# Performance work log

Hardware: AMD Instinct MI355X
Metric: run time of the kernel (lower is better)

## Reference

```python
import jax, jax.numpy as jnp
import numpy as np

B, H, W, C, F = 32, 32, 32, 256, 64
K_NEIGH = 32  # L1 pixel-distance cutoff used for the static mask


def _distance_mask(h, w, k):
    # coords: [hw, 2] of (y, x); L1 pixel distances, normalized by max(h, w)
    ys, xs = jnp.meshgrid(jnp.arange(h), jnp.arange(w), indexing='ij')
    coords = jnp.stack([ys, xs], axis=-1).reshape(-1, 2).astype(jnp.float32)
    diff = jnp.abs(coords[:, None, :] - coords[None, :, :]).sum(-1)  # [hw, hw], == cdist p=1
    dist = diff / float(max(h, w))
    return jnp.where(diff <= k, dist, 0.0)


def setup_inputs() -> dict:
    key = jax.random.key(0)
    ks = jax.random.split(key, 7)
    return {
        'feature_map': jax.random.normal(ks[0], (B, H, W, C), dtype=jnp.float32),
        'emb_W': jax.random.normal(ks[1], (F, C), dtype=jnp.float32) * (1.0 / np.sqrt(C)),
        'emb_b': jax.random.normal(ks[2], (F,), dtype=jnp.float32) * 0.01,
        'attn_W': jax.random.normal(ks[3], (C, C), dtype=jnp.float32) * (1.0 / np.sqrt(C)),
        'attn_b': jax.random.normal(ks[4], (C,), dtype=jnp.float32) * 0.01,
        'thr_W': jax.random.normal(ks[5], (1, C), dtype=jnp.float32) * (1.0 / np.sqrt(C)),
        'thr_b': jax.random.normal(ks[6], (1,), dtype=jnp.float32) * 0.01,
        'layer': 0,
    }


def reference(feature_map, emb_W, emb_b, attn_W, attn_b, thr_W, thr_b, layer):
    b, h, w, c = feature_map.shape
    hw = h * w
    x = feature_map.reshape(b, hw, c)  # row-major (y, x) flatten, matches torch view

    # 1x1 conv -> per-pixel linear: instance embeddings [b, hw, F]
    emb = jnp.einsum('bnc,fc->bnf', x, emb_W) + emb_b

    # squared Euclidean pairwise distances (cdist p=2, then squared)
    sq = jnp.sum(emb * emb, axis=-1)  # [b, hw]
    d2 = jnp.maximum(sq[:, :, None] + sq[:, None, :]
                     - 2.0 * jnp.einsum('bnf,bmf->bnm', emb, emb), 0.0)

    mask = _distance_mask(h, w, K_NEIGH)  # [hw, hw] static buffer
    sim = jax.nn.softmax(jnp.exp(-d2) - (1.0 - mask), axis=-1)  # [b, hw, hw]

    # shortcut = attention_conv(feature_map): [b, hw, c]
    shortcut = jnp.einsum('bnc,dc->bnd', x, attn_W) + attn_b

    # per-pixel learned threshold: [b, hw]
    Tinst = (jnp.einsum('bnc,oc->bno', shortcut, thr_W) + thr_b)[..., 0]

    A = jax.nn.softmax(jnp.maximum(sim - Tinst[:, None, :], 0.0), axis=-1)

    # bmm: out[b, i, c] = sum_j shortcut[b, j, c] * A[b, i, j]
    attn_out = jnp.einsum('bjc,bij->bic', shortcut, A)

    res = (x + attn_out).reshape(b, h, w, c)
    return res
```

## Files before the change

kernel.cpp:

```cpp
#include <hip/hip_runtime.h>
#include <hip/hip_bf16.h>


typedef short bf16x8 __attribute__((ext_vector_type(8)));
typedef float f32x4 __attribute__((ext_vector_type(4)));

#define LOG2E 1.4426950408889634f

__device__ __forceinline__ unsigned short f2bf(float f) {
  unsigned u = __float_as_uint(f);
  u += 0x7fffu + ((u >> 16) & 1u);
  return (unsigned short)(u >> 16);
}
__device__ __forceinline__ float bf2f(unsigned short h) {
  return __uint_as_float(((unsigned)h) << 16);
}
__device__ __forceinline__ unsigned pack2(float a, float b) {
  return (unsigned)f2bf(a) | ((unsigned)f2bf(b) << 16);
}
__device__ __forceinline__ unsigned cvtpk(float lo, float hi) {
  unsigned r;
  asm("v_cvt_pk_bf16_f32 %0, %1, %2" : "=v"(r) : "v"(lo), "v"(hi));
  return r;
}
__device__ __forceinline__ float exp2x(float x) {
  float r;
  asm("v_exp_f32 %0, %1" : "=v"(r) : "v"(x));
  return r;
}
__device__ __forceinline__ f32x4 mfma16(bf16x8 a, bf16x8 b, f32x4 c) {
  return __builtin_amdgcn_mfma_f32_16x16x32_bf16(a, b, c, 0, 0, 0);
}
__device__ __forceinline__ int iabs(int v) { return v < 0 ? -v : v; }
__device__ __forceinline__ void load_lds16(const void* g, void* l) {
  __builtin_amdgcn_global_load_lds(
      (const __attribute__((address_space(1))) unsigned int*)g,
      (__attribute__((address_space(3))) unsigned int*)l, 16, 0, 0);
}

__device__ __forceinline__ float e_chain(float g, float nsq2i, float sq2j,
                                         int diff) {
  float w2 = fminf(fmaf(2.f * LOG2E, g, nsq2i - sq2j), 0.f);
  float fd = (float)diff;
  float fs = (diff <= 32) ? fd : 0.f;
  return exp2x(fmaf(exp2x(w2), LOG2E, fmaf(fs, LOG2E / 32.f, -LOG2E)));
}

__global__ __launch_bounds__(256) void k_prep(const float* __restrict__ embW,
                                              const float* __restrict__ attnW,
                                              unsigned short* __restrict__ Wb) {
  const int i = (blockIdx.x * 256 + threadIdx.x) * 4;
  float4 v = (i < 16384) ? *(const float4*)(embW + i)
                         : *(const float4*)(attnW + (i - 16384));
  ushort4 p; p.x = f2bf(v.x); p.y = f2bf(v.y); p.z = f2bf(v.z); p.w = f2bf(v.w);
  *(ushort4*)(Wb + i) = p;
}

__global__ __launch_bounds__(256) void k_lin(const float* __restrict__ x,
                                             const unsigned short* __restrict__ Wb,
                                             const float* __restrict__ embB,
                                             const float* __restrict__ attnB,
                                             const float* __restrict__ thrW,
                                             const float* __restrict__ thrB,
                                             unsigned short* __restrict__ embb,
                                             float* __restrict__ sq2,
                                             unsigned short* __restrict__ scT,
                                             float* __restrict__ T2out) {
  __shared__ union {
    struct { unsigned short xs[64][40]; unsigned short ws[320][40]; } a;
    unsigned short St[256][72];
  } sm;
  const int t = threadIdx.x;
  const int Mbase = blockIdx.x * 64;
  const int lane = t & 63, wave = t >> 6;
  const int wm = wave >> 1, wn = wave & 1;
  const int l15 = lane & 15, quad = lane >> 4;

  f32x4 acc[2][10] = {};
  for (int k0 = 0; k0 < 256; k0 += 32) {
    {
      int row = t >> 2, c0 = (t & 3) * 8;
      const float* src = x + (size_t)(Mbase + row) * 256 + k0 + c0;
      float4 a = *(const float4*)src;
      float4 b = *(const float4*)(src + 4);
      uint4 p; p.x = pack2(a.x, a.y); p.y = pack2(a.z, a.w);
      p.z = pack2(b.x, b.y); p.w = pack2(b.z, b.w);
      *(uint4*)&sm.a.xs[row][c0] = p;
    }
    {
      const unsigned short* wsrc = Wb + (size_t)t * 256 + k0;
      for (int s = 0; s < 4; s++)
        *(uint4*)&sm.a.ws[t][s * 8] = *(const uint4*)(wsrc + s * 8);
      if (t < 64) {
        const unsigned short* wsrc2 = Wb + (size_t)(256 + t) * 256 + k0;
        for (int s = 0; s < 4; s++)
          *(uint4*)&sm.a.ws[256 + t][s * 8] = *(const uint4*)(wsrc2 + s * 8);
      }
    }
    __syncthreads();
    bf16x8 af[2];
    af[0] = *(const bf16x8*)&sm.a.xs[wm * 32 + l15][quad * 8];
    af[1] = *(const bf16x8*)&sm.a.xs[wm * 32 + 16 + l15][quad * 8];
    for (int nt = 0; nt < 10; nt++) {
      bf16x8 bfr = *(const bf16x8*)&sm.a.ws[wn * 160 + nt * 16 + l15][quad * 8];
      acc[0][nt] = mfma16(af[0], bfr, acc[0][nt]);
      acc[1][nt] = mfma16(af[1], bfr, acc[1][nt]);
    }
    __syncthreads();
  }

  if (wn == 0) {
    float sp[2][4] = {{0.f,0.f,0.f,0.f},{0.f,0.f,0.f,0.f}};
    for (int rt = 0; rt < 2; rt++)
      for (int nt = 0; nt < 4; nt++) {
        int n = nt * 16 + l15;
        float bias = embB[n];
        for (int r = 0; r < 4; r++) {
          float v = acc[rt][nt][r] + bias;
          unsigned short hb = f2bf(v);
          int row = wm * 32 + rt * 16 + quad * 4 + r;
          embb[(size_t)(Mbase + row) * 64 + n] = hb;
          float vf = bf2f(hb);
          sp[rt][r] += vf * vf;
        }
      }
    for (int m = 8; m >= 1; m >>= 1)
      for (int rt = 0; rt < 2; rt++)
        for (int r = 0; r < 4; r++)
          sp[rt][r] += __shfl_xor(sp[rt][r], m);
    if (l15 == 0)
      for (int rt = 0; rt < 2; rt++)
        for (int r = 0; r < 4; r++)
          sq2[Mbase + wm * 32 + rt * 16 + quad * 4 + r] = sp[rt][r] * LOG2E;
  }

  for (int rt = 0; rt < 2; rt++)
    for (int nt = 0; nt < 10; nt++) {
      int n = wn * 160 + nt * 16 + l15;
      if (n < 64) continue;
      int c = n - 64;
      float bias = attnB[c];
      for (int r = 0; r < 4; r++) {
        float v = acc[rt][nt][r] + bias;
        sm.St[c][wm * 32 + rt * 16 + quad * 4 + r] = f2bf(v);
      }
    }
  __syncthreads();

  const int b = Mbase >> 10, jbase = Mbase & 1023;
  {
    unsigned short* dst = scT + ((size_t)b * 256 + t) * 1024 + jbase;
    for (int s = 0; s < 8; s++)
      *(uint4*)(dst + s * 8) = *(const uint4*)&sm.St[t][s * 8];
  }
  {
    float tp = 0.f;
    int j = t >> 2, cs = (t & 3) * 64;
    for (int c = 0; c < 64; c++)
      tp += bf2f(sm.St[cs + c][j]) * thrW[cs + c];
    tp += __shfl_xor(tp, 1);
    tp += __shfl_xor(tp, 2);
    if ((t & 3) == 0) T2out[Mbase + j] = (tp + thrB[0]) * LOG2E;
  }
}

__global__ __launch_bounds__(256) void k_out2(const unsigned short* __restrict__ embb,
                                              const float* __restrict__ sq2,
                                              const float* __restrict__ T2,
                                              const unsigned short* __restrict__ scT,
                                              const float* __restrict__ x,
                                              float* __restrict__ out) {
  __shared__ unsigned short Kb[2][32 * 64];
  __shared__ unsigned short Sb[2][1024 * 8];
  __shared__ unsigned short Pb[2][64 * 40];
  __shared__ float zbuf[64];
  const int t = threadIdx.x, lane = t & 63, w = t >> 6;
  const int l15 = lane & 15, quad = lane >> 4;
  const int b = blockIdx.x & 31, rt = blockIdx.x >> 5;
  const unsigned short* eb = embb + (size_t)b * 1024 * 64;
  const float* sq2b = sq2 + b * 1024;
  const float* T2b = T2 + b * 1024;

  const int qrow = w * 16 + l15;
  const int gi = rt * 64 + qrow;
  bf16x8 qf0 = *(const bf16x8*)(eb + (size_t)gi * 64 + quad * 8);
  bf16x8 qf1 = *(const bf16x8*)(eb + (size_t)gi * 64 + 32 + quad * 8);
  const float nsq2q = -sq2b[gi];
  const int yi = gi >> 5, xi = gi & 31;

  const int krow = t >> 3;
  const int kchunk = (t & 7) ^ (krow & 7);
  const int sw = l15 & 7;
  const unsigned short* srow = scT + ((size_t)b * 256 + t) * 1024;

#define STAGE_K(bufi, j0s)                                                   \
  load_lds16(eb + (size_t)((j0s) + krow) * 64 + kchunk * 8, &Kb[bufi][t * 8])
#define STAGE_S(bufi, j0s)                                                   \
  do {                                                                       \
    load_lds16(srow + (j0s), &Sb[bufi][(0 * 256 + t) * 8]);                  \
    load_lds16(srow + (j0s) + 8, &Sb[bufi][(1 * 256 + t) * 8]);              \
    load_lds16(srow + (j0s) + 16, &Sb[bufi][(2 * 256 + t) * 8]);             \
    load_lds16(srow + (j0s) + 24, &Sb[bufi][(3 * 256 + t) * 8]);             \
  } while (0)

  STAGE_K(0, 0);
  __syncthreads();
  float rp = 0.f;
  #pragma unroll 2
  for (int it = 0; it < 32; ++it) {
    const int cur = it & 1;
    const int j0 = it * 32;
    if (it < 31) STAGE_K(cur ^ 1, j0 + 32);
    bf16x8 kf00 = *(const bf16x8*)&Kb[cur][(l15) * 64 + ((0 * 4 + quad) ^ sw) * 8];
    bf16x8 kf01 = *(const bf16x8*)&Kb[cur][(l15) * 64 + ((1 * 4 + quad) ^ sw) * 8];
    bf16x8 kf10 = *(const bf16x8*)&Kb[cur][(16 + l15) * 64 + ((0 * 4 + quad) ^ sw) * 8];
    bf16x8 kf11 = *(const bf16x8*)&Kb[cur][(16 + l15) * 64 + ((1 * 4 + quad) ^ sw) * 8];
    f32x4 g0 = {0.f, 0.f, 0.f, 0.f}, g1 = {0.f, 0.f, 0.f, 0.f};
    g0 = mfma16(kf00, qf0, g0);
    g0 = mfma16(kf01, qf1, g0);
    g1 = mfma16(kf10, qf0, g1);
    g1 = mfma16(kf11, qf1, g1);
    #pragma unroll
    for (int jt = 0; jt < 2; ++jt) {
      const f32x4 g = jt ? g1 : g0;
      const int jg = j0 + jt * 16 + quad * 4;
      const float4 s4 = *(const float4*)(sq2b + jg);
      const int dy = iabs(yi - (jg >> 5));
      const int dxa = xi - (jg & 31);
      float e0 = e_chain(g[0], nsq2q, s4.x, dy + iabs(dxa));
      float e1 = e_chain(g[1], nsq2q, s4.y, dy + iabs(dxa - 1));
      float e2 = e_chain(g[2], nsq2q, s4.z, dy + iabs(dxa - 2));
      float e3 = e_chain(g[3], nsq2q, s4.w, dy + iabs(dxa - 3));
      rp += (e0 + e1) + (e2 + e3);
    }
    if (it < 31) __syncthreads();
  }
  rp += __shfl_xor(rp, 16);
  rp += __shfl_xor(rp, 32);
  const float invR2 = LOG2E / rp;

  STAGE_K(0, 0);
  STAGE_S(0, 0);
  __syncthreads();

  f32x4 acc[4][4] = {};
  float zloc = 0.f;
  #pragma unroll 2
  for (int it = 0; it < 32; ++it) {
    const int cur = it & 1;
    const int j0 = it * 32;
    if (it < 31) { STAGE_K(cur ^ 1, j0 + 32); STAGE_S(cur ^ 1, j0 + 32); }

    bf16x8 kf00 = *(const bf16x8*)&Kb[cur][(l15) * 64 + ((0 * 4 + quad) ^ sw) * 8];
    bf16x8 kf01 = *(const bf16x8*)&Kb[cur][(l15) * 64 + ((1 * 4 + quad) ^ sw) * 8];
    bf16x8 kf10 = *(const bf16x8*)&Kb[cur][(16 + l15) * 64 + ((0 * 4 + quad) ^ sw) * 8];
    bf16x8 kf11 = *(const bf16x8*)&Kb[cur][(16 + l15) * 64 + ((1 * 4 + quad) ^ sw) * 8];
    f32x4 g0 = {0.f, 0.f, 0.f, 0.f}, g1 = {0.f, 0.f, 0.f, 0.f};
    g0 = mfma16(kf00, qf0, g0);
    g0 = mfma16(kf01, qf1, g0);
    g1 = mfma16(kf10, qf0, g1);
    g1 = mfma16(kf11, qf1, g1);

    #pragma unroll
    for (int jt = 0; jt < 2; ++jt) {
      const f32x4 g = jt ? g1 : g0;
      const int jg = j0 + jt * 16 + quad * 4;
      const float4 s4 = *(const float4*)(sq2b + jg);
      const float4 t4 = *(const float4*)(T2b + jg);
      const int dy = iabs(yi - (jg >> 5));
      const int dxa = xi - (jg & 31);
      float e0 = e_chain(g[0], nsq2q, s4.x, dy + iabs(dxa));
      float e1 = e_chain(g[1], nsq2q, s4.y, dy + iabs(dxa - 1));
      float e2 = e_chain(g[2], nsq2q, s4.z, dy + iabs(dxa - 2));
      float e3 = e_chain(g[3], nsq2q, s4.w, dy + iabs(dxa - 3));
      float u0 = exp2x(fmaxf(fmaf(e0, invR2, -t4.x), 0.f));
      float u1 = exp2x(fmaxf(fmaf(e1, invR2, -t4.y), 0.f));
      float u2 = exp2x(fmaxf(fmaf(e2, invR2, -t4.z), 0.f));
      float u3 = exp2x(fmaxf(fmaf(e3, invR2, -t4.w), 0.f));
      unsigned pk0 = cvtpk(u0, u1);
      unsigned pk1 = cvtpk(u2, u3);
      zloc += __uint_as_float(pk0 << 16) + __uint_as_float(pk0 & 0xffff0000u);
      zloc += __uint_as_float(pk1 << 16) + __uint_as_float(pk1 & 0xffff0000u);
      uint2 pk; pk.x = pk0; pk.y = pk1;
      *(uint2*)&Pb[cur][qrow * 40 + jt * 16 + quad * 4] = pk;
    }
    __syncthreads();

    bf16x8 af[4], bfv[4];
    #pragma unroll
    for (int i = 0; i < 4; i++)
      af[i] = *(const bf16x8*)&Pb[cur][(i * 16 + l15) * 40 + quad * 8];
    #pragma unroll
    for (int n = 0; n < 4; n++)
      bfv[n] = *(const bf16x8*)&Sb[cur][(quad * 256 + w * 64 + n * 16 + l15) * 8];
    #pragma unroll
    for (int i = 0; i < 4; i++)
      #pragma unroll
      for (int n = 0; n < 4; n++)
        acc[i][n] = mfma16(af[i], bfv[n], acc[i][n]);
  }
#undef STAGE_K
#undef STAGE_S

  zloc += __shfl_xor(zloc, 16);
  zloc += __shfl_xor(zloc, 32);
  if (quad == 0) zbuf[qrow] = zloc;
  __syncthreads();

  #pragma unroll
  for (int i = 0; i < 4; i++) {
    const int rowl = i * 16 + quad * 4;
    float iz[4];
    #pragma unroll
    for (int r = 0; r < 4; r++) iz[r] = 1.f / zbuf[rowl + r];
    const int grow = b * 1024 + rt * 64 + rowl;
    #pragma unroll
    for (int n = 0; n < 4; n++) {
      const int c = w * 64 + n * 16 + l15;
      #pragma unroll
      for (int r = 0; r < 4; r++) {
        size_t idx = (size_t)(grow + r) * 256 + c;
        out[idx] = x[idx] + acc[i][n][r] * iz[r];
      }
    }
  }
}

extern "C" void kernel_launch(void* const* d_in, const int* in_sizes, int n_in,
                              void* d_out, int out_size, void* d_ws, size_t ws_size,
                              hipStream_t stream) {
  const float* x     = (const float*)d_in[0];
  const float* embW  = (const float*)d_in[1];
  const float* embB  = (const float*)d_in[2];
  const float* attnW = (const float*)d_in[3];
  const float* attnB = (const float*)d_in[4];
  const float* thrW  = (const float*)d_in[5];
  const float* thrB  = (const float*)d_in[6];
  float* out = (float*)d_out;

  char* ws = (char*)d_ws;
  unsigned short* embb = (unsigned short*)(ws);
  unsigned short* scT  = (unsigned short*)(ws + (4ull << 20));
  unsigned short* Wb   = (unsigned short*)(ws + (20ull << 20));
  float* sq2 = (float*)(ws + (84ull << 20));
  float* T2  = (float*)(ws + (84ull << 20) + (128ull << 10));

  k_prep<<<80, 256, 0, stream>>>(embW, attnW, Wb);
  k_lin<<<512, 256, 0, stream>>>(x, Wb, embB, attnB, thrW, thrB, embb, sq2, scT, T2);
  k_out2<<<512, 256, 0, stream>>>(embb, sq2, T2, scT, x, out);
}
```

Baseline: 198.0 us.

## Cache first-pass exp values in registers as packed bf16 to skip recompute

```diff
diff --git a/kernel.cpp b/kernel.cpp
--- a/kernel.cpp
+++ b/kernel.cpp
@@ -203,10 +203,11 @@
     load_lds16(srow + (j0s) + 24, &Sb[bufi][(3 * 256 + t) * 8]);             \
   } while (0)
 
+  unsigned epk[128];
   STAGE_K(0, 0);
   __syncthreads();
   float rp = 0.f;
-  #pragma unroll 2
+  #pragma unroll
   for (int it = 0; it < 32; ++it) {
     const int cur = it & 1;
     const int j0 = it * 32;
@@ -232,6 +233,8 @@
       float e2 = e_chain(g[2], nsq2q, s4.z, dy + iabs(dxa - 2));
       float e3 = e_chain(g[3], nsq2q, s4.w, dy + iabs(dxa - 3));
       rp += (e0 + e1) + (e2 + e3);
+      epk[it * 4 + jt * 2 + 0] = cvtpk(e0, e1);
+      epk[it * 4 + jt * 2 + 1] = cvtpk(e2, e3);
     }
     if (it < 31) __syncthreads();
   }
@@ -239,40 +242,27 @@
   rp += __shfl_xor(rp, 32);
   const float invR2 = LOG2E / rp;
 
-  STAGE_K(0, 0);
   STAGE_S(0, 0);
   __syncthreads();
 
   f32x4 acc[4][4] = {};
   float zloc = 0.f;
-  #pragma unroll 2
+  #pragma unroll
   for (int it = 0; it < 32; ++it) {
     const int cur = it & 1;
     const int j0 = it * 32;
-    if (it < 31) { STAGE_K(cur ^ 1, j0 + 32); STAGE_S(cur ^ 1, j0 + 32); }
-
-    bf16x8 kf00 = *(const bf16x8*)&Kb[cur][(l15) * 64 + ((0 * 4 + quad) ^ sw) * 8];
-    bf16x8 kf01 = *(const bf16x8*)&Kb[cur][(l15) * 64 + ((1 * 4 + quad) ^ sw) * 8];
-    bf16x8 kf10 = *(const bf16x8*)&Kb[cur][(16 + l15) * 64 + ((0 * 4 + quad) ^ sw) * 8];
-    bf16x8 kf11 = *(const bf16x8*)&Kb[cur][(16 + l15) * 64 + ((1 * 4 + quad) ^ sw) * 8];
-    f32x4 g0 = {0.f, 0.f, 0.f, 0.f}, g1 = {0.f, 0.f, 0.f, 0.f};
-    g0 = mfma16(kf00, qf0, g0);
-    g0 = mfma16(kf01, qf1, g0);
-    g1 = mfma16(kf10, qf0, g1);
-    g1 = mfma16(kf11, qf1, g1);
+    if (it < 31) STAGE_S(cur ^ 1, j0 + 32);
 
     #pragma unroll
     for (int jt = 0; jt < 2; ++jt) {
-      const f32x4 g = jt ? g1 : g0;
       const int jg = j0 + jt * 16 + quad * 4;
-      const float4 s4 = *(const float4*)(sq2b + jg);
       const float4 t4 = *(const float4*)(T2b + jg);
-      const int dy = iabs(yi - (jg >> 5));
-      const int dxa = xi - (jg & 31);
-      float e0 = e_chain(g[0], nsq2q, s4.x, dy + iabs(dxa));
-      float e1 = e_chain(g[1], nsq2q, s4.y, dy + iabs(dxa - 1));
-      float e2 = e_chain(g[2], nsq2q, s4.z, dy + iabs(dxa - 2));
-      float e3 = e_chain(g[3], nsq2q, s4.w, dy + iabs(dxa - 3));
+      const unsigned p0 = epk[it * 4 + jt * 2 + 0];
+      const unsigned p1 = epk[it * 4 + jt * 2 + 1];
+      const float e0 = __uint_as_float(p0 << 16);
+      const float e1 = __uint_as_float(p0 & 0xffff0000u);
+      const float e2 = __uint_as_float(p1 << 16);
+      const float e3 = __uint_as_float(p1 & 0xffff0000u);
       float u0 = exp2x(fmaxf(fmaf(e0, invR2, -t4.x), 0.f));
       float u1 = exp2x(fmaxf(fmaf(e1, invR2, -t4.y), 0.f));
       float u2 = exp2x(fmaxf(fmaf(e2, invR2, -t4.z), 0.f));
```

Result: slower. 235.9 us (+19.1%).

## Halve query tile, split key range across waves, read keys directly from global

Applied to the files above, without the earlier changes.

```diff
diff --git a/kernel.cpp b/kernel.cpp
--- a/kernel.cpp
+++ b/kernel.cpp
@@ -164,37 +164,32 @@
   }
 }
 
-__global__ __launch_bounds__(256) void k_out2(const unsigned short* __restrict__ embb,
-                                              const float* __restrict__ sq2,
-                                              const float* __restrict__ T2,
-                                              const unsigned short* __restrict__ scT,
-                                              const float* __restrict__ x,
-                                              float* __restrict__ out) {
-  __shared__ unsigned short Kb[2][32 * 64];
+__global__ __launch_bounds__(256, 4) void k_out2(const unsigned short* __restrict__ embb,
+                                                 const float* __restrict__ sq2,
+                                                 const float* __restrict__ T2,
+                                                 const unsigned short* __restrict__ scT,
+                                                 const float* __restrict__ x,
+                                                 float* __restrict__ out) {
   __shared__ unsigned short Sb[2][1024 * 8];
-  __shared__ unsigned short Pb[2][64 * 40];
-  __shared__ float zbuf[64];
+  __shared__ unsigned short Pb[2][32 * 40];
+  __shared__ float rtmp[2][32];
+  __shared__ float zsum[2][32];
   const int t = threadIdx.x, lane = t & 63, w = t >> 6;
   const int l15 = lane & 15, quad = lane >> 4;
+  const int wr = w & 1, wj = w >> 1;
   const int b = blockIdx.x & 31, rt = blockIdx.x >> 5;
   const unsigned short* eb = embb + (size_t)b * 1024 * 64;
   const float* sq2b = sq2 + b * 1024;
   const float* T2b = T2 + b * 1024;
 
-  const int qrow = w * 16 + l15;
-  const int gi = rt * 64 + qrow;
+  const int qrow = wr * 16 + l15;
+  const int gi = rt * 32 + qrow;
   bf16x8 qf0 = *(const bf16x8*)(eb + (size_t)gi * 64 + quad * 8);
   bf16x8 qf1 = *(const bf16x8*)(eb + (size_t)gi * 64 + 32 + quad * 8);
   const float nsq2q = -sq2b[gi];
   const int yi = gi >> 5, xi = gi & 31;
 
-  const int krow = t >> 3;
-  const int kchunk = (t & 7) ^ (krow & 7);
-  const int sw = l15 & 7;
   const unsigned short* srow = scT + ((size_t)b * 256 + t) * 1024;
-
-#define STAGE_K(bufi, j0s)                                                   \
-  load_lds16(eb + (size_t)((j0s) + krow) * 64 + kchunk * 8, &Kb[bufi][t * 8])
 #define STAGE_S(bufi, j0s)                                                   \
   do {                                                                       \
     load_lds16(srow + (j0s), &Sb[bufi][(0 * 256 + t) * 8]);                  \
@@ -203,23 +198,24 @@
     load_lds16(srow + (j0s) + 24, &Sb[bufi][(3 * 256 + t) * 8]);             \
   } while (0)
 
-  STAGE_K(0, 0);
-  __syncthreads();
+  STAGE_S(0, 0);
+
   float rp = 0.f;
+  const int jq = wj * 512;
   #pragma unroll 2
-  for (int it = 0; it < 32; ++it) {
-    const int cur = it & 1;
-    const int j0 = it * 32;
-    if (it < 31) STAGE_K(cur ^ 1, j0 + 32);
-    bf16x8 kf00 = *(const bf16x8*)&Kb[cur][(l15) * 64 + ((0 * 4 + quad) ^ sw) * 8];
-    bf16x8 kf01 = *(const bf16x8*)&Kb[cur][(l15) * 64 + ((1 * 4 + quad) ^ sw) * 8];
-    bf16x8 kf10 = *(const bf16x8*)&Kb[cur][(16 + l15) * 64 + ((0 * 4 + quad) ^ sw) * 8];
-    bf16x8 kf11 = *(const bf16x8*)&Kb[cur][(16 + l15) * 64 + ((1 * 4 + quad) ^ sw) * 8];
+  for (int it = 0; it < 16; ++it) {
+    const int j0 = jq + it * 32;
+    const unsigned short* jr0 = eb + (size_t)(j0 + l15) * 64;
+    const unsigned short* jr1 = eb + (size_t)(j0 + 16 + l15) * 64;
+    bf16x8 a00 = *(const bf16x8*)(jr0 + quad * 8);
+    bf16x8 a01 = *(const bf16x8*)(jr0 + 32 + quad * 8);
+    bf16x8 a10 = *(const bf16x8*)(jr1 + quad * 8);
+    bf16x8 a11 = *(const bf16x8*)(jr1 + 32 + quad * 8);
     f32x4 g0 = {0.f, 0.f, 0.f, 0.f}, g1 = {0.f, 0.f, 0.f, 0.f};
-    g0 = mfma16(kf00, qf0, g0);
-    g0 = mfma16(kf01, qf1, g0);
-    g1 = mfma16(kf10, qf0, g1);
-    g1 = mfma16(kf11, qf1, g1);
+    g0 = mfma16(a00, qf0, g0);
+    g0 = mfma16(a01, qf1, g0);
+    g1 = mfma16(a10, qf0, g1);
+    g1 = mfma16(a11, qf1, g1);
     #pragma unroll
     for (int jt = 0; jt < 2; ++jt) {
       const f32x4 g = jt ? g1 : g0;
@@ -233,38 +229,29 @@
       float e3 = e_chain(g[3], nsq2q, s4.w, dy + iabs(dxa - 3));
       rp += (e0 + e1) + (e2 + e3);
     }
-    if (it < 31) __syncthreads();
   }
   rp += __shfl_xor(rp, 16);
   rp += __shfl_xor(rp, 32);
-  const float invR2 = LOG2E / rp;
-
-  STAGE_K(0, 0);
-  STAGE_S(0, 0);
+  if (quad == 0) rtmp[wj][qrow] = rp;
   __syncthreads();
-
-  f32x4 acc[4][4] = {};
+  const float invR2 = LOG2E / (rtmp[0][qrow] + rtmp[1][qrow]);
+
+  f32x4 acc[2][4] = {};
   float zloc = 0.f;
   #pragma unroll 2
   for (int it = 0; it < 32; ++it) {
     const int cur = it & 1;
     const int j0 = it * 32;
-    if (it < 31) { STAGE_K(cur ^ 1, j0 + 32); STAGE_S(cur ^ 1, j0 + 32); }
-
-    bf16x8 kf00 = *(const bf16x8*)&Kb[cur][(l15) * 64 + ((0 * 4 + quad) ^ sw) * 8];
-    bf16x8 kf01 = *(const bf16x8*)&Kb[cur][(l15) * 64 + ((1 * 4 + quad) ^ sw) * 8];
-    bf16x8 kf10 = *(const bf16x8*)&Kb[cur][(16 + l15) * 64 + ((0 * 4 + quad) ^ sw) * 8];
-    bf16x8 kf11 = *(const bf16x8*)&Kb[cur][(16 + l15) * 64 + ((1 * 4 + quad) ^ sw) * 8];
-    f32x4 g0 = {0.f, 0.f, 0.f, 0.f}, g1 = {0.f, 0.f, 0.f, 0.f};
-    g0 = mfma16(kf00, qf0, g0);
-    g0 = mfma16(kf01, qf1, g0);
-    g1 = mfma16(kf10, qf0, g1);
-    g1 = mfma16(kf11, qf1, g1);
-
-    #pragma unroll
-    for (int jt = 0; jt < 2; ++jt) {
-      const f32x4 g = jt ? g1 : g0;
-      const int jg = j0 + jt * 16 + quad * 4;
+
+    const int jp = j0 + wj * 16;
+    const unsigned short* jr = eb + (size_t)(jp + l15) * 64;
+    bf16x8 a0 = *(const bf16x8*)(jr + quad * 8);
+    bf16x8 a1 = *(const bf16x8*)(jr + 32 + quad * 8);
+    f32x4 g = {0.f, 0.f, 0.f, 0.f};
+    g = mfma16(a0, qf0, g);
+    g = mfma16(a1, qf1, g);
+    {
+      const int jg = jp + quad * 4;
       const float4 s4 = *(const float4*)(sq2b + jg);
       const float4 t4 = *(const float4*)(T2b + jg);
       const int dy = iabs(yi - (jg >> 5));
@@ -282,38 +269,40 @@
       zloc += __uint_as_float(pk0 << 16) + __uint_as_float(pk0 & 0xffff0000u);
       zloc += __uint_as_float(pk1 << 16) + __uint_as_float(pk1 & 0xffff0000u);
       uint2 pk; pk.x = pk0; pk.y = pk1;
-      *(uint2*)&Pb[cur][qrow * 40 + jt * 16 + quad * 4] = pk;
+      *(uint2*)&Pb[cur][qrow * 40 + wj * 16 + quad * 4] = pk;
     }
     __syncthreads();
 
-    bf16x8 af[4], bfv[4];
-    #pragma unroll
-    for (int i = 0; i < 4; i++)
+    if (it < 31) STAGE_S(cur ^ 1, j0 + 32);
+
+    bf16x8 af[2], bfv[4];
+    #pragma unroll
+    for (int i = 0; i < 2; i++)
       af[i] = *(const bf16x8*)&Pb[cur][(i * 16 + l15) * 40 + quad * 8];
     #pragma unroll
     for (int n = 0; n < 4; n++)
       bfv[n] = *(const bf16x8*)&Sb[cur][(quad * 256 + w * 64 + n * 16 + l15) * 8];
     #pragma unroll
-    for (int i = 0; i < 4; i++)
+    for (int i = 0; i < 2; i++)
       #pragma unroll
       for (int n = 0; n < 4; n++)
         acc[i][n] = mfma16(af[i], bfv[n], acc[i][n]);
   }
-#undef STAGE_K
 #undef STAGE_S
 
   zloc += __shfl_xor(zloc, 16);
   zloc += __shfl_xor(zloc, 32);
-  if (quad == 0) zbuf[qrow] = zloc;
+  if (quad == 0) zsum[wj][qrow] = zloc;
   __syncthreads();
 
   #pragma unroll
-  for (int i = 0; i < 4; i++) {
+  for (int i = 0; i < 2; i++) {
     const int rowl = i * 16 + quad * 4;
     float iz[4];
     #pragma unroll
-    for (int r = 0; r < 4; r++) iz[r] = 1.f / zbuf[rowl + r];
-    const int grow = b * 1024 + rt * 64 + rowl;
+    for (int r = 0; r < 4; r++)
+      iz[r] = 1.f / (zsum[0][rowl + r] + zsum[1][rowl + r]);
+    const int grow = b * 1024 + rt * 32 + rowl;
     #pragma unroll
     for (int n = 0; n < 4; n++) {
       const int c = w * 64 + n * 16 + l15;
@@ -347,5 +336,5 @@
 
   k_prep<<<80, 256, 0, stream>>>(embW, attnW, Wb);
   k_lin<<<512, 256, 0, stream>>>(x, Wb, embB, attnB, thrW, thrB, embb, sq2, scT, T2);
-  k_out2<<<512, 256, 0, stream>>>(embb, sq2, T2, scT, x, out);
-}
+  k_out2<<<1024, 256, 0, stream>>>(embb, sq2, T2, scT, x, out);
+}
```

New measurement: 259.4 us. 1.31x slower.
